# Performance work log

Measured on AMD Instinct MI355X. Metric: run time of the kernel, lower is better.

The kernel has to match this reference:

```python
import jax, jax.numpy as jnp
import numpy as np

BETA = 10.0
EPS = 1e-6


def setup_inputs() -> dict:
    key = jax.random.key(0)
    k0, k1 = jax.random.split(key)
    f0 = jax.random.normal(k0, (4, 256, 64, 64), dtype=jnp.float32)
    f1 = jax.random.normal(k1, (4, 256, 64, 64), dtype=jnp.float32)
    return {"f0": f0, "f1": f1}


def _l2norm(x, axis):
    norm = jnp.sqrt(jnp.sum(x * x, axis=axis, keepdims=True))
    return x / jnp.maximum(norm, EPS)


def reference(f0, f1):
    B, C, Ha, Wa = f0.shape
    _, _, Hb, Wb = f1.shape
    # [B, HaWa, C] and [B, HbWb, C]
    a = f0.reshape(B, C, Ha * Wa).transpose(0, 2, 1)
    b = f1.reshape(B, C, Hb * Wb).transpose(0, 2, 1)
    a = _l2norm(a, axis=2)
    b = _l2norm(b, axis=2)
    # cosine similarity scaled by beta: [B, HaWa, HbWb]
    sim = jnp.einsum('bnc,bmc->bnm', a, b) * BETA
    attn = jax.nn.softmax(sim, axis=2)
    # target coords (x, y) of image1 grid: [HbWb, 2]
    ys = jnp.arange(Hb, dtype=f0.dtype)
    xs = jnp.arange(Wb, dtype=f0.dtype)
    yy, xx = jnp.meshgrid(ys, xs, indexing='ij')
    coords = jnp.stack([xx.reshape(-1), yy.reshape(-1)], axis=1)
    tgt = jnp.einsum('bnm,mk->bnk', attn, coords)
    warp_c = tgt.reshape(B, Ha, Wa, 2)
    cert_c = jnp.max(attn, axis=2).reshape(B, Ha, Wa)
    return (warp_c, cert_c)
```

## Files before the change

kernel.cpp:

```cpp
#include <hip/hip_runtime.h>
#include <hip/hip_bf16.h>

#define BETA_LOG2E 14.426950408889634f
#define EPSN 1e-6f

typedef __bf16 bf16x8 __attribute__((ext_vector_type(8)));
typedef float  f32x4  __attribute__((ext_vector_type(4)));

static __device__ inline unsigned short f2bf(float f) {
    __hip_bfloat16 h = __float2bfloat16(f);
    return __builtin_bit_cast(unsigned short, h);
}
static __device__ inline float bf2f(unsigned short u) {
    unsigned int b = ((unsigned int)u) << 16;
    return __builtin_bit_cast(float, b);
}

__global__ __launch_bounds__(256) void k_norm_transpose(
    const float* __restrict__ f0, const float* __restrict__ f1,
    unsigned short* __restrict__ aT, unsigned short* __restrict__ bT)
{
    __shared__ unsigned short tile[32 * 256];
    __shared__ float partial[32][32];
    __shared__ float inv_l[32];

    int idx   = blockIdx.x;
    int which = idx >> 9;
    int rem   = idx & 511;
    int b     = rem >> 7;
    int n0    = (rem & 127) * 32;
    const float* src = which ? f1 : f0;
    unsigned short* dst = which ? bT : aT;
    float scale = which ? 1.0f : BETA_LOG2E;

    int t  = threadIdx.x;
    int nq = t & 7;
    int cg = t >> 3;

    const float* sp = src + ((size_t)(b * 256 + cg * 8)) * 4096 + n0 + nq * 4;

    f32x4 ss = {0.f, 0.f, 0.f, 0.f};
    unsigned int pk[4][4];
#pragma unroll
    for (int i = 0; i < 8; ++i) {
        f32x4 v = *reinterpret_cast<const f32x4*>(sp + (size_t)i * 4096);
        ss += v * v;
#pragma unroll
        for (int j = 0; j < 4; ++j) {
            unsigned int h = f2bf(v[j]);
            if (i & 1) pk[j][i >> 1] |= h << 16;
            else       pk[j][i >> 1]  = h;
        }
    }
#pragma unroll
    for (int j = 0; j < 4; ++j) {
        int n = nq * 4 + j;
        *reinterpret_cast<uint4*>(&tile[n * 256 + cg * 8]) =
            *reinterpret_cast<const uint4*>(pk[j]);
    }
    *reinterpret_cast<f32x4*>(&partial[cg][nq * 4]) = ss;
    __syncthreads();
    if (t < 32) {
        float s = 0.f;
#pragma unroll
        for (int k = 0; k < 32; ++k) s += partial[k][t];
        inv_l[t] = scale / fmaxf(sqrtf(s), EPSN);
    }
    __syncthreads();

#pragma unroll
    for (int it = 0; it < 4; ++it) {
        int n  = it * 8 + (t >> 5);
        int cb = t & 31;
        uint4 v = *reinterpret_cast<const uint4*>(&tile[n * 256 + cb * 8]);
        float inv = inv_l[n];
        unsigned int o[4];
#pragma unroll
        for (int k = 0; k < 4; ++k) {
            unsigned int u = (&v.x)[k];
            unsigned short lo = f2bf(bf2f((unsigned short)(u & 0xffffu)) * inv);
            unsigned short hi = f2bf(bf2f((unsigned short)(u >> 16)) * inv);
            o[k] = (unsigned int)lo | ((unsigned int)hi << 16);
        }
        *reinterpret_cast<uint4*>(&dst[((size_t)(b * 4096 + n0 + n)) * 256 + cb * 8]) =
            *reinterpret_cast<const uint4*>(o);
    }
}

__global__ __launch_bounds__(256) void k_flash(
    const unsigned short* __restrict__ aT, const unsigned short* __restrict__ bT,
    float* __restrict__ stats)
{
    __shared__ unsigned short kb[2 * 64 * 256];

    int idx   = blockIdx.x;
    int xcd   = idx & 7;
    int batch = xcd >> 1;
    int sub   = ((idx >> 3) << 1) | (xcd & 1);
    int qt    = sub >> 2;
    int ks    = sub & 3;

    int t    = threadIdx.x;
    int w    = t >> 6;
    int lane = t & 63;
    int quad = lane >> 4;
    int l15  = lane & 15;
    int q0w  = qt * 128 + w * 32;
    int k0   = ks * 1024;

    bf16x8 afrag[2][8];
#pragma unroll
    for (int s = 0; s < 2; ++s) {
        const unsigned short* ap =
            aT + ((size_t)(batch * 4096 + q0w + s * 16 + l15)) * 256 + quad * 8;
#pragma unroll
        for (int kk = 0; kk < 8; ++kk)
            afrag[s][kk] = *reinterpret_cast<const bf16x8*>(ap + kk * 32);
    }

    int s7 = l15 & 7;
    int offs[8];
#pragma unroll
    for (int kk = 0; kk < 8; ++kk) offs[kk] = (((quad + 4 * kk) ^ s7) << 3);

    int krem = 2 * w + (lane >> 5);
    int goff = krem * 256 + (((lane & 31) ^ (krem & 7)) << 3);

    float Z[8], V[8], U[8], Sm[8];
#pragma unroll
    for (int i = 0; i < 8; ++i) { Z[i] = 0.f; V[i] = 0.f; U[i] = 0.f; Sm[i] = -1e30f; }

    const unsigned short* gkbase = bT + ((size_t)(batch * 4096 + k0)) * 256;

#define STAGE(CH, BUFHW)                                                        \
    {                                                                           \
        const unsigned short* gsp = gkbase + (size_t)(CH) * 16384 + goff;       \
        unsigned short* lp0 = kb + (BUFHW) + w * 512;                           \
        _Pragma("unroll")                                                       \
        for (int i = 0; i < 8; ++i)                                             \
            __builtin_amdgcn_global_load_lds(                                   \
                (const __attribute__((address_space(1))) void*)(gsp + i * 2048),\
                (__attribute__((address_space(3))) void*)(lp0 + i * 2048),      \
                16, 0, 0);                                                      \
    }

    STAGE(0, 0);
    __syncthreads();
    int bufOff = 0;

    for (int ch = 0; ch < 16; ++ch) {
        if (ch < 15) STAGE(ch + 1, bufOff ^ 16384);

#pragma unroll
        for (int nt = 0; nt < 4; ++nt) {
            f32x4 acc0 = {0.f, 0.f, 0.f, 0.f};
            f32x4 acc1 = {0.f, 0.f, 0.f, 0.f};
            const unsigned short* lp = kb + bufOff + (nt * 16 + l15) * 256;
#pragma unroll
            for (int kk = 0; kk < 8; ++kk) {
                bf16x8 bfrag = *reinterpret_cast<const bf16x8*>(lp + offs[kk]);
                acc0 = __builtin_amdgcn_mfma_f32_16x16x32_bf16(afrag[0][kk], bfrag, acc0, 0, 0, 0);
                acc1 = __builtin_amdgcn_mfma_f32_16x16x32_bf16(afrag[1][kk], bfrag, acc1, 0, 0, 0);
            }
#pragma unroll
            for (int r = 0; r < 4; ++r) {
                float p0 = exp2f(acc0[r]);
                Z[r]  += p0;
                Sm[r]  = fmaxf(Sm[r], acc0[r]);
                float p1 = exp2f(acc1[r]);
                Z[4 + r]  += p1;
                Sm[4 + r]  = fmaxf(Sm[4 + r], acc1[r]);
            }
            if (nt < 3) {
#pragma unroll
                for (int i = 0; i < 8; ++i) V[i] += Z[i];
            }
        }
#pragma unroll
        for (int i = 0; i < 8; ++i) U[i] += Z[i];
        __syncthreads();
        bufOff ^= 16384;
    }
#undef STAGE

    float l15f = (float)l15;
#pragma unroll
    for (int i = 0; i < 8; ++i) V[i] = l15f * Z[i] - 16.0f * V[i];

#pragma unroll
    for (int i = 0; i < 8; ++i) {
#pragma unroll
        for (int m = 1; m <= 8; m <<= 1) {
            Z[i]  += __shfl_xor(Z[i], m);
            V[i]  += __shfl_xor(V[i], m);
            U[i]  += __shfl_xor(U[i], m);
            Sm[i]  = fmaxf(Sm[i], __shfl_xor(Sm[i], m));
        }
    }
    if (l15 == 0) {
        float kyc = 16.0f * (float)(ks + 1);
#pragma unroll
        for (int s = 0; s < 2; ++s)
#pragma unroll
            for (int r = 0; r < 4; ++r) {
                int q = q0w + s * 16 + quad * 4 + r;
                int i = s * 4 + r;
                float Sx = V[i] + 48.0f * U[i];
                float Sy = kyc * Z[i] - U[i];
                f32x4 st = {Z[i], Sx, Sy, exp2f(Sm[i])};
                *reinterpret_cast<f32x4*>(&stats[((size_t)(batch * 4096 + q) * 4 + ks) * 4]) = st;
            }
    }
}

__global__ __launch_bounds__(256) void k_finalize(
    const float* __restrict__ stats, float* __restrict__ out)
{
    int q = blockIdx.x * 256 + threadIdx.x;
    const f32x4* s = reinterpret_cast<const f32x4*>(stats + (size_t)q * 16);
    f32x4 a0 = s[0], a1 = s[1], a2 = s[2], a3 = s[3];
    float Z  = a0.x + a1.x + a2.x + a3.x;
    float Sx = a0.y + a1.y + a2.y + a3.y;
    float Sy = a0.z + a1.z + a2.z + a3.z;
    float Pm = fmaxf(fmaxf(a0.w, a1.w), fmaxf(a2.w, a3.w));
    float invZ = 1.0f / Z;
    out[q * 2 + 0]  = Sx * invZ;
    out[q * 2 + 1]  = Sy * invZ;
    out[32768 + q]  = Pm * invZ;
}

extern "C" void kernel_launch(void* const* d_in, const int* in_sizes, int n_in,
                              void* d_out, int out_size, void* d_ws, size_t ws_size,
                              hipStream_t stream)
{
    const float* f0 = (const float*)d_in[0];
    const float* f1 = (const float*)d_in[1];
    unsigned short* aT = (unsigned short*)d_ws;
    unsigned short* bT = aT + (size_t)4 * 4096 * 256;
    float* stats = (float*)(bT + (size_t)4 * 4096 * 256);
    float* out = (float*)d_out;

    hipLaunchKernelGGL(k_norm_transpose, dim3(1024), dim3(256), 0, stream, f0, f1, aT, bT);
    hipLaunchKernelGGL(k_flash,          dim3(512),  dim3(256), 0, stream, aT, bT, stats);
    hipLaunchKernelGGL(k_finalize,       dim3(64),   dim3(256), 0, stream, stats, out);
}
```

Before: 122.3 us.

## Enlarge flash query tile to 256 rows and split keys eight ways

Each workgroup now handles 256 query rows (64 per wave, four MFMA row groups) against 512 keys instead of 128 rows against 1024 keys. Every K tile staged in LDS is therefore reused by twice as many query rows, which halves K-side global and LDS traffic per unit of compute. The stats buffer and finalize kernel are widened to combine eight key splits, and launch_bounds asks for two blocks per CU. In exchange, register pressure roughly doubles (32 A fragments and 64 accumulator scalars), which risks spilling or lower occupancy, and the extra key splits add reduction work in finalize.

```diff
diff --git a/kernel.cpp b/kernel.cpp
--- a/kernel.cpp
+++ b/kernel.cpp
@@ -87,7 +87,7 @@
     }
 }
 
-__global__ __launch_bounds__(256) void k_flash(
+__global__ __launch_bounds__(256, 2) void k_flash(
     const unsigned short* __restrict__ aT, const unsigned short* __restrict__ bT,
     float* __restrict__ stats)
 {
@@ -99,18 +99,21 @@
     int sub   = ((idx >> 3) << 1) | (xcd & 1);
     int qt    = sub >> 2;
     int ks    = sub & 3;
+    sub   = ((idx >> 3) << 1) | (xcd & 1);
+    qt    = sub >> 3;
+    ks    = sub & 7;
 
     int t    = threadIdx.x;
     int w    = t >> 6;
     int lane = t & 63;
     int quad = lane >> 4;
     int l15  = lane & 15;
-    int q0w  = qt * 128 + w * 32;
-    int k0   = ks * 1024;
-
-    bf16x8 afrag[2][8];
-#pragma unroll
-    for (int s = 0; s < 2; ++s) {
+    int q0w  = qt * 256 + w * 64;
+    int k0   = ks * 512;
+
+    bf16x8 afrag[4][8];
+#pragma unroll
+    for (int s = 0; s < 4; ++s) {
         const unsigned short* ap =
             aT + ((size_t)(batch * 4096 + q0w + s * 16 + l15)) * 256 + quad * 8;
 #pragma unroll
@@ -126,9 +129,9 @@
     int krem = 2 * w + (lane >> 5);
     int goff = krem * 256 + (((lane & 31) ^ (krem & 7)) << 3);
 
-    float Z[8], V[8], U[8], Sm[8];
-#pragma unroll
-    for (int i = 0; i < 8; ++i) { Z[i] = 0.f; V[i] = 0.f; U[i] = 0.f; Sm[i] = -1e30f; }
+    float Z[16], V[16], U[16], Sm[16];
+#pragma unroll
+    for (int i = 0; i < 16; ++i) { Z[i] = 0.f; V[i] = 0.f; U[i] = 0.f; Sm[i] = -1e30f; }
 
     const unsigned short* gkbase = bT + ((size_t)(batch * 4096 + k0)) * 256;
 
@@ -148,36 +151,42 @@
     __syncthreads();
     int bufOff = 0;
 
-    for (int ch = 0; ch < 16; ++ch) {
-        if (ch < 15) STAGE(ch + 1, bufOff ^ 16384);
+    for (int ch = 0; ch < 8; ++ch) {
+        if (ch < 7) STAGE(ch + 1, bufOff ^ 16384);
 
 #pragma unroll
         for (int nt = 0; nt < 4; ++nt) {
             f32x4 acc0 = {0.f, 0.f, 0.f, 0.f};
             f32x4 acc1 = {0.f, 0.f, 0.f, 0.f};
+            f32x4 acc2 = {0.f, 0.f, 0.f, 0.f};
+            f32x4 acc3 = {0.f, 0.f, 0.f, 0.f};
             const unsigned short* lp = kb + bufOff + (nt * 16 + l15) * 256;
 #pragma unroll
             for (int kk = 0; kk < 8; ++kk) {
                 bf16x8 bfrag = *reinterpret_cast<const bf16x8*>(lp + offs[kk]);
                 acc0 = __builtin_amdgcn_mfma_f32_16x16x32_bf16(afrag[0][kk], bfrag, acc0, 0, 0, 0);
                 acc1 = __builtin_amdgcn_mfma_f32_16x16x32_bf16(afrag[1][kk], bfrag, acc1, 0, 0, 0);
+                acc2 = __builtin_amdgcn_mfma_f32_16x16x32_bf16(afrag[2][kk], bfrag, acc2, 0, 0, 0);
+                acc3 = __builtin_amdgcn_mfma_f32_16x16x32_bf16(afrag[3][kk], bfrag, acc3, 0, 0, 0);
             }
 #pragma unroll
             for (int r = 0; r < 4; ++r) {
                 float p0 = exp2f(acc0[r]);
-                Z[r]  += p0;
-                Sm[r]  = fmaxf(Sm[r], acc0[r]);
+                Z[r]      += p0;  Sm[r]      = fmaxf(Sm[r],      acc0[r]);
                 float p1 = exp2f(acc1[r]);
-                Z[4 + r]  += p1;
-                Sm[4 + r]  = fmaxf(Sm[4 + r], acc1[r]);
+                Z[4 + r]  += p1;  Sm[4 + r]  = fmaxf(Sm[4 + r],  acc1[r]);
+                float p2 = exp2f(acc2[r]);
+                Z[8 + r]  += p2;  Sm[8 + r]  = fmaxf(Sm[8 + r],  acc2[r]);
+                float p3 = exp2f(acc3[r]);
+                Z[12 + r] += p3;  Sm[12 + r] = fmaxf(Sm[12 + r], acc3[r]);
             }
             if (nt < 3) {
 #pragma unroll
-                for (int i = 0; i < 8; ++i) V[i] += Z[i];
-            }
-        }
-#pragma unroll
-        for (int i = 0; i < 8; ++i) U[i] += Z[i];
+                for (int i = 0; i < 16; ++i) V[i] += Z[i];
+            }
+        }
+#pragma unroll
+        for (int i = 0; i < 16; ++i) U[i] += Z[i];
         __syncthreads();
         bufOff ^= 16384;
     }
@@ -185,10 +194,10 @@
 
     float l15f = (float)l15;
 #pragma unroll
-    for (int i = 0; i < 8; ++i) V[i] = l15f * Z[i] - 16.0f * V[i];
-
-#pragma unroll
-    for (int i = 0; i < 8; ++i) {
+    for (int i = 0; i < 16; ++i) V[i] = l15f * Z[i] - 16.0f * V[i];
+
+#pragma unroll
+    for (int i = 0; i < 16; ++i) {
 #pragma unroll
         for (int m = 1; m <= 8; m <<= 1) {
             Z[i]  += __shfl_xor(Z[i], m);
@@ -198,9 +207,9 @@
         }
     }
     if (l15 == 0) {
-        float kyc = 16.0f * (float)(ks + 1);
-#pragma unroll
-        for (int s = 0; s < 2; ++s)
+        float kyc = 8.0f * (float)(ks + 1);
+#pragma unroll
+        for (int s = 0; s < 4; ++s)
 #pragma unroll
             for (int r = 0; r < 4; ++r) {
                 int q = q0w + s * 16 + quad * 4 + r;
@@ -208,7 +217,7 @@
                 float Sx = V[i] + 48.0f * U[i];
                 float Sy = kyc * Z[i] - U[i];
                 f32x4 st = {Z[i], Sx, Sy, exp2f(Sm[i])};
-                *reinterpret_cast<f32x4*>(&stats[((size_t)(batch * 4096 + q) * 4 + ks) * 4]) = st;
+                *reinterpret_cast<f32x4*>(&stats[((size_t)(batch * 4096 + q) * 8 + ks) * 4]) = st;
             }
     }
 }
@@ -217,12 +226,13 @@
     const float* __restrict__ stats, float* __restrict__ out)
 {
     int q = blockIdx.x * 256 + threadIdx.x;
-    const f32x4* s = reinterpret_cast<const f32x4*>(stats + (size_t)q * 16);
-    f32x4 a0 = s[0], a1 = s[1], a2 = s[2], a3 = s[3];
-    float Z  = a0.x + a1.x + a2.x + a3.x;
-    float Sx = a0.y + a1.y + a2.y + a3.y;
-    float Sy = a0.z + a1.z + a2.z + a3.z;
-    float Pm = fmaxf(fmaxf(a0.w, a1.w), fmaxf(a2.w, a3.w));
+    const f32x4* s = reinterpret_cast<const f32x4*>(stats + (size_t)q * 32);
+    float Z = 0.f, Sx = 0.f, Sy = 0.f, Pm = 0.f;
+#pragma unroll
+    for (int k = 0; k < 8; ++k) {
+        f32x4 a = s[k];
+        Z += a.x; Sx += a.y; Sy += a.z; Pm = fmaxf(Pm, a.w);
+    }
     float invZ = 1.0f / Z;
     out[q * 2 + 0]  = Sx * invZ;
     out[q * 2 + 1]  = Sy * invZ;
```

After: 170.1 us. 1.39x slower.
